# Kernel optimization log

Measured on AMD Instinct MI355X. Metric: run time of the kernel, lower is better.

Reference implementation:

```python
import jax, jax.numpy as jnp
import numpy as np
from functools import partial

N = 100000
E = 1600000
F_IN, F_HID, F_OUT = 128, 128, 64


def setup_inputs() -> dict:
    key = jax.random.key(0)
    ks = jax.random.split(key, 10)
    x = jax.random.normal(ks[0], (N, F_IN), dtype=jnp.float32)
    edge_index = jax.random.randint(ks[1], (2, E), 0, N, dtype=jnp.int64)
    edge_attr = jax.random.uniform(ks[2], (E,), dtype=jnp.float32)
    # GCNConv params: Linear(in, out, bias=False) weight + separate bias
    def glorot(k, fan_in, fan_out):
        lim = jnp.sqrt(6.0 / (fan_in + fan_out))
        return jax.random.uniform(k, (fan_in, fan_out), minval=-lim, maxval=lim, dtype=jnp.float32)
    return {
        "x": x, "edge_index": edge_index, "edge_attr": edge_attr,
        "W1": glorot(ks[3], F_IN, F_HID),  "b1": jnp.zeros((F_HID,), jnp.float32),
        "W2": glorot(ks[4], F_HID, F_HID), "b2": jnp.zeros((F_HID,), jnp.float32),
        "W3": glorot(ks[5], F_HID, F_OUT), "b3": jnp.zeros((F_OUT,), jnp.float32),
    }


def _gcn_norm(src, dst, ew, n):
    # PyG gcn_norm: add self-loops with weight 1, symmetric normalization.
    loop = jnp.arange(n, dtype=src.dtype)
    src_f = jnp.concatenate([src, loop])
    dst_f = jnp.concatenate([dst, loop])
    ew_f = jnp.concatenate([ew, jnp.ones((n,), ew.dtype)])
    deg = jax.ops.segment_sum(ew_f, dst_f, num_segments=n)
    dinv = jnp.where(deg > 0, jax.lax.rsqrt(deg), 0.0)
    norm = dinv[src_f] * ew_f * dinv[dst_f]  # [E+N]
    return src_f, dst_f, norm


def _gcn_conv(x, W, b, src_f, dst_f, norm, n):
    h = x @ W  # [N, out]
    msg = norm[:, None] * h[src_f]  # gather + per-edge scale
    out = jax.ops.segment_sum(msg, dst_f, num_segments=n)  # scatter-add
    return out + b


def reference(x, edge_index, edge_attr, W1, b1, W2, b2, W3, b3):
    n = x.shape[0]
    src, dst = edge_index[0], edge_index[1]
    src_f, dst_f, norm = _gcn_norm(src, dst, edge_attr, n)
    h = jax.nn.relu(_gcn_conv(x, W1, b1, src_f, dst_f, norm, n))
    h = jax.nn.relu(_gcn_conv(h, W2, b2, src_f, dst_f, norm, n))
    out = _gcn_conv(h, W3, b3, src_f, dst_f, norm, n)
    return jax.nn.log_softmax(out, axis=-1)
```

## Files before the change

kernel.cpp:

```cpp
#include <hip/hip_runtime.h>

typedef unsigned short ushortT;
typedef unsigned int uintT;
typedef unsigned long long ullT;
typedef __attribute__((ext_vector_type(8))) short bf16x8;
typedef __attribute__((ext_vector_type(4))) float f32x4;

#define NBUCK 391
#define EPB   4096
#define NBEB  391
#define BSLOT 4608
#define NCONV 3125

union H16 { ushortT u; _Float16 h; };

__device__ __forceinline__ float bf2f(uintT u16) {
    return __uint_as_float(u16 << 16);
}
__device__ __forceinline__ float bflo(uintT u) {
    return __uint_as_float(u << 16);
}
__device__ __forceinline__ float bfhi(uintT u) {
    return __uint_as_float(u & 0xffff0000u);
}
__device__ __forceinline__ ushortT f2bf(float f) {
    unsigned int u = __float_as_uint(f);
    unsigned int r = (u + 0x7fffu + ((u >> 16) & 1u)) >> 16;
    return (ushortT)r;
}

#define ACC8(U, W) \
    acc[0] = fmaf(W, bflo(U.x), acc[0]); acc[1] = fmaf(W, bfhi(U.x), acc[1]); \
    acc[2] = fmaf(W, bflo(U.y), acc[2]); acc[3] = fmaf(W, bfhi(U.y), acc[3]); \
    acc[4] = fmaf(W, bflo(U.z), acc[4]); acc[5] = fmaf(W, bfhi(U.z), acc[5]); \
    acc[6] = fmaf(W, bflo(U.w), acc[6]); acc[7] = fmaf(W, bfhi(U.w), acc[7]);


__device__ __forceinline__ void twist_body(const float* W, ushortT* Wt, int K, int C, int idx) {
    if (idx < K * C) {
        int k = idx / C, c = idx - k * C;
        Wt[c * K + k] = f2bf(W[idx]);
    }
}

__device__ __forceinline__ void conv_body(const float* x, ushortT* xb, int idx) {
    const float4* xp = reinterpret_cast<const float4*>(x) + (size_t)idx * 2;
    float4 a = xp[0], b = xp[1];
    uint4 o;
    o.x = (uintT)f2bf(a.x) | ((uintT)f2bf(a.y) << 16);
    o.y = (uintT)f2bf(a.z) | ((uintT)f2bf(a.w) << 16);
    o.z = (uintT)f2bf(b.x) | ((uintT)f2bf(b.y) << 16);
    o.w = (uintT)f2bf(b.z) | ((uintT)f2bf(b.w) << 16);
    *reinterpret_cast<uint4*>(xb + (size_t)idx * 8) = o;
}

template <int C>
__device__ __forceinline__ void gemm_body(const ushortT* A, const ushortT* Wt,
                                          ushortT* outp, int nrows, int bid, int tid) {
    const int K = 128;
    int wv = tid >> 6;
    int ln = tid & 63;
    int row0 = (bid * 4 + wv) * 16;
    if (row0 >= nrows) return;
    int rA = ln & 15;
    int kg = ln >> 4;
    int rowA = row0 + rA;
    bool okA = rowA < nrows;

    bf16x8 af[4];
    #pragma unroll
    for (int kb = 0; kb < 4; ++kb) {
        if (okA) af[kb] = *(const bf16x8*)(A + (size_t)rowA * K + kb * 32 + kg * 8);
        else     af[kb] = (bf16x8)(short)0;
    }

    int colB = ln & 15;
    f32x4 acc[C / 16];
    #pragma unroll
    for (int nt = 0; nt < C / 16; ++nt) acc[nt] = (f32x4)0.0f;
    #pragma unroll
    for (int nt = 0; nt < C / 16; ++nt) {
        int c = nt * 16 + colB;
        #pragma unroll
        for (int kb = 0; kb < 4; ++kb) {
            bf16x8 bfr = *(const bf16x8*)(Wt + c * K + kb * 32 + kg * 8);
            acc[nt] = __builtin_amdgcn_mfma_f32_16x16x32_bf16(af[kb], bfr, acc[nt], 0, 0, 0);
        }
    }
    #pragma unroll
    for (int nt = 0; nt < C / 16; ++nt) {
        #pragma unroll
        for (int r = 0; r < 4; ++r) {
            int rowC = row0 + (ln >> 4) * 4 + r;
            if (rowC < nrows) outp[(size_t)rowC * C + nt * 16 + colB] = f2bf(acc[nt][r]);
        }
    }
}

__global__ __launch_bounds__(512) void k_sort_twist(const int* src, const int* dst, const float* ew,
                                                    int* bucket_count, ullT* erec, int e,
                                                    const float* W1, ushortT* Wt1,
                                                    const float* W2, ushortT* Wt2,
                                                    const float* W3, ushortT* Wt3,
                                                    const float* x, ushortT* xb) {
    __shared__ ullT srec[EPB];
    __shared__ int  gaddr[EPB];
    __shared__ int  hist[512];
    __shared__ int  adj[NBUCK];
    int blk = blockIdx.x, t = threadIdx.x;
    if (blk >= NBEB) {
        int tb = blk - NBEB;
        if (tb < 32)      twist_body(W1, Wt1, 128, 128, tb * 512 + t);
        else if (tb < 64) twist_body(W2, Wt2, 128, 128, (tb - 32) * 512 + t);
        else if (tb < 80) twist_body(W3, Wt3, 128, 64, (tb - 64) * 512 + t);
        else              conv_body(x, xb, (tb - 80) * 512 + t);
        return;
    }
    hist[t] = 0;
    __syncthreads();
    int base = blk * EPB;
    for (int j = t; j < EPB; j += 512) {
        int i = base + j;
        if (i < e) atomicAdd(&hist[dst[i] >> 8], 1);
    }
    __syncthreads();
    int myc = hist[t];
    for (int off = 1; off < 512; off <<= 1) {
        int x2 = 0; if (t >= off) x2 = hist[t - off];
        __syncthreads();
        if (t >= off) hist[t] += x2;
        __syncthreads();
    }
    int lb = (t == 0) ? 0 : hist[t - 1];
    __syncthreads();
    hist[t] = lb;
    if (t < NBUCK) {
        int gb = 0;
        if (myc > 0) gb = atomicAdd(&bucket_count[t], myc);
        adj[t] = t * BSLOT + gb - lb;
    }
    __syncthreads();
    for (int j = t; j < EPB; j += 512) {
        int i = base + j;
        if (i < e) {
            int d = dst[i];
            int b = d >> 8;
            int pos = atomicAdd(&hist[b], 1);
            H16 cv; cv.h = (_Float16)ew[i];
            ullT rec = ((ullT)(uintT)src[i] << 24) | ((ullT)(uintT)(d & 255) << 16) | (ullT)cv.u;
            srec[pos] = rec;
            int ga = adj[b] + pos;
            int lim = b * BSLOT + BSLOT - 1;
            gaddr[pos] = ga <= lim ? ga : lim;
        }
    }
    __syncthreads();
    int m = e - base; if (m > EPB) m = EPB;
    for (int k = t; k < m; k += 512) {
        erec[(size_t)gaddr[k]] = srec[k];
    }
}

__global__ __launch_bounds__(256) void k_bucket_gemm1(const ullT* erec,
                                                      const int* bucket_count,
                                                      uintT* entries, float* dinv, int* counts, int n,
                                                      const ushortT* xb, const ushortT* Wt1,
                                                      ushortT* hw1) {
    __shared__ int cnt[256];
    __shared__ uintT wsum[256];
    int blk = blockIdx.x, t = threadIdx.x;
    if (blk < NBUCK) {
        int b = blk;
        cnt[t] = 0; wsum[t] = 0;
        __syncthreads();
        int beg = b * BSLOT, m = bucket_count[b];
        if (m > BSLOT) m = BSLOT;
        for (int j = t; j < m; j += 256) {
            ullT rec = erec[(size_t)beg + j];
            int dlow = (int)((rec >> 16) & 255);
            ushortT hu = (ushortT)(rec & 0xffffu);
            int slot = atomicAdd(&cnt[dlow], 1);
            H16 cv; cv.u = hu;
            atomicAdd(&wsum[dlow], (uintT)__float2uint_rn((float)cv.h * 16777216.0f));
            if (slot < 64) {
                uintT s = (uintT)(rec >> 24);
                entries[((size_t)b * 256 + dlow) * 64 + slot] = (s << 15) | (uintT)hu;
            }
        }
        __syncthreads();
        int node = b * 256 + t;
        if (node < n) {
            float sum = (float)wsum[t] * (1.0f / 16777216.0f);
            dinv[node] = rsqrtf(1.0f + sum);
            int c = cnt[t];
            counts[node] = c > 64 ? 64 : c;
        }
    } else {
        gemm_body<128>(xb, Wt1, hw1, n, blk - NBUCK, t);
    }
}

template <int C>
__global__ __launch_bounds__(256) void k_agg_gemm(const char* hwb, const float* dinv,
                                                  const int* counts, const uintT* entries,
                                                  const float* bias, const ushortT* Wt,
                                                  ushortT* outp, int n) {
    __shared__ ullT wp[4][64];
    __shared__ uintT rows[16][64];
    int wv = threadIdx.x >> 6, ln = threadIdx.x & 63;
    int tile0 = blockIdx.x * 16;
    int lg = ln & 15;
    int gp = ln >> 4;

    float wfac4[4], wsrc4[4];
    int   cnt4[4];
    uintT ent4[4];
    #pragma unroll
    for (int nn = 0; nn < 4; ++nn) {
        int i = tile0 + wv * 4 + nn;
        wfac4[nn] = dinv[i];
        cnt4[nn]  = counts[i];
        ent4[nn]  = entries[(size_t)i * 64 + ln];
        wsrc4[nn] = dinv[(int)(ent4[nn] >> 15)];
    }

    const char* lane_base = hwb + (size_t)(lg * 16);

    #pragma unroll
    for (int nn = 0; nn < 4; ++nn) {
        int r = wv * 4 + nn;
        int i = tile0 + r;
        float wfac = wfac4[nn];
        int cnt = cnt4[nn];
        int cntp = (cnt + 7) & ~7;
        uintT ent = ent4[nn];
        H16 cv; cv.u = (ushortT)(ent & 0x7fffu);
        float w_l = (ln < cnt) ? wsrc4[nn] * (float)cv.h * wfac : 0.f;
        uintT soff = (ln < cnt) ? ((ent >> 15) << 8) : 0u;
        wp[wv][ln] = ((ullT)__float_as_uint(w_l) << 32) | (ullT)soff;
        const ullT* wpw = wp[wv];

        uint4 uself = *(const uint4*)(lane_base + (size_t)i * 256);

        float acc[8];
        #pragma unroll
        for (int j = 0; j < 8; ++j) acc[j] = 0.f;

        ullT pa = wpw[gp], pb = wpw[4 + gp];
        uint4 ua = *(const uint4*)(lane_base + (uintT)pa);
        uint4 ub = *(const uint4*)(lane_base + (uintT)pb);
        for (int e = 8; e < cntp; e += 8) {
            ullT pa2 = wpw[e + gp], pb2 = wpw[e + 4 + gp];
            uint4 ua2 = *(const uint4*)(lane_base + (uintT)pa2);
            uint4 ub2 = *(const uint4*)(lane_base + (uintT)pb2);
            float wa = __uint_as_float((uintT)(pa >> 32));
            float wb = __uint_as_float((uintT)(pb >> 32));
            ACC8(ua, wa)
            ACC8(ub, wb)
            pa = pa2; pb = pb2; ua = ua2; ub = ub2;
        }
        {
            float wa = __uint_as_float((uintT)(pa >> 32));
            float wb = __uint_as_float((uintT)(pb >> 32));
            ACC8(ua, wa)
            ACC8(ub, wb)
        }

        #pragma unroll
        for (int j = 0; j < 8; ++j) {
            acc[j] += __shfl_xor(acc[j], 16);
            acc[j] += __shfl_xor(acc[j], 32);
        }
        float selfw = wfac * wfac;
        ACC8(uself, selfw)

        float a0 = (gp & 1) ? ((gp & 2) ? acc[6] : acc[2]) : ((gp & 2) ? acc[4] : acc[0]);
        float a1 = (gp & 1) ? ((gp & 2) ? acc[7] : acc[3]) : ((gp & 2) ? acc[5] : acc[1]);
        int d = lg * 4 + gp;
        float2 bs = *(const float2*)(bias + 2 * d);
        a0 = fmaxf(a0 + bs.x, 0.f);
        a1 = fmaxf(a1 + bs.y, 0.f);
        uintT packed = (uintT)f2bf(a0) | ((uintT)f2bf(a1) << 16);
        rows[r][((d * 4) ^ ((r & 7) << 4)) >> 2] = packed;
    }
    __syncthreads();

    {
        int rA = ln & 15;
        int kg = ln >> 4;
        int colB = ln & 15;
        const char* rbase = (const char*)&rows[0][0];
        bf16x8 af[4];
        #pragma unroll
        for (int kb = 0; kb < 4; ++kb) {
            int byteoff = (kb * 64 + kg * 16) ^ ((rA & 7) << 4);
            af[kb] = *(const bf16x8*)(rbase + rA * 256 + byteoff);
        }
        const int NS = C / 64;
        #pragma unroll
        for (int s = 0; s < NS; ++s) {
            int nt = wv * NS + s;
            f32x4 gac = (f32x4)0.0f;
            int c = nt * 16 + colB;
            #pragma unroll
            for (int kb = 0; kb < 4; ++kb) {
                bf16x8 bfr = *(const bf16x8*)(Wt + c * 128 + kb * 32 + kg * 8);
                gac = __builtin_amdgcn_mfma_f32_16x16x32_bf16(af[kb], bfr, gac, 0, 0, 0);
            }
            #pragma unroll
            for (int r = 0; r < 4; ++r) {
                int rowC = tile0 + kg * 4 + r;
                outp[(size_t)rowC * C + nt * 16 + colB] = f2bf(gac[r]);
            }
        }
    }
}

__global__ __launch_bounds__(256) void k_agg_softmax(const char* hwb, const float* dinv,
                                                     const int* counts, const uintT* entries,
                                                     const float* bias, float* outp, int n) {
    __shared__ ullT wp[4][64];
    int wv = threadIdx.x >> 6, ln = threadIdx.x & 63;
    int i = blockIdx.x * 4 + wv;
    if (i >= n) return;
    int lg = ln & 7;
    int gp = ln >> 3;

    float wfac = dinv[i];
    int cnt = counts[i];
    int cntp = (cnt + 7) & ~7;
    uintT ent = entries[(size_t)i * 64 + ln];
    int s_l = (ln < cnt) ? (int)(ent >> 15) : 0;
    H16 cv; cv.u = (ushortT)(ent & 0x7fffu);
    float w_l = (ln < cnt) ? dinv[s_l] * (float)cv.h * wfac : 0.f;
    wp[wv][ln] = ((ullT)__float_as_uint(w_l) << 32) | (ullT)((uintT)s_l << 7);
    const ullT* wpw = wp[wv];

    const char* lane_base = hwb + (size_t)(lg * 16);
    uint4 uself = *(const uint4*)(lane_base + (size_t)i * 128);

    float acc[8];
    #pragma unroll
    for (int j = 0; j < 8; ++j) acc[j] = 0.f;

    ullT paA = wpw[gp];
    uint4 uaA = *(const uint4*)(lane_base + (uintT)paA);
    bool hasB = cntp > 8;
    ullT paB = 0;
    uint4 uaB = {0, 0, 0, 0};
    if (hasB) {
        paB = wpw[8 + gp];
        uaB = *(const uint4*)(lane_base + (uintT)paB);
    }
    for (int e = 16; e < cntp; e += 8) {
        ullT paC = wpw[e + gp];
        uint4 uaC = *(const uint4*)(lane_base + (uintT)paC);
        float wa = __uint_as_float((uintT)(paA >> 32));
        ACC8(uaA, wa)
        paA = paB; uaA = uaB;
        paB = paC; uaB = uaC;
    }
    {
        float wa = __uint_as_float((uintT)(paA >> 32));
        ACC8(uaA, wa)
    }
    if (hasB) {
        float wa = __uint_as_float((uintT)(paB >> 32));
        ACC8(uaB, wa)
    }

    #pragma unroll
    for (int j = 0; j < 8; ++j) {
        acc[j] += __shfl_xor(acc[j], 8);
        acc[j] += __shfl_xor(acc[j], 16);
        acc[j] += __shfl_xor(acc[j], 32);
    }
    float selfw = wfac * wfac;
    ACC8(uself, selfw)

    float4 bsa = *(const float4*)(bias + lg * 8);
    float4 bsb = *(const float4*)(bias + lg * 8 + 4);
    acc[0] += bsa.x; acc[1] += bsa.y; acc[2] += bsa.z; acc[3] += bsa.w;
    acc[4] += bsb.x; acc[5] += bsb.y; acc[6] += bsb.z; acc[7] += bsb.w;

    float m = acc[0];
    #pragma unroll
    for (int j = 1; j < 8; ++j) m = fmaxf(m, acc[j]);
    m = fmaxf(m, __shfl_xor(m, 1));
    m = fmaxf(m, __shfl_xor(m, 2));
    m = fmaxf(m, __shfl_xor(m, 4));
    float s = 0.f;
    #pragma unroll
    for (int j = 0; j < 8; ++j) s += __expf(acc[j] - m);
    s += __shfl_xor(s, 1);
    s += __shfl_xor(s, 2);
    s += __shfl_xor(s, 4);
    float ls = m + __logf(s);

    float v0 = (gp & 1) ? acc[4] : acc[0];
    float v1 = (gp & 1) ? acc[5] : acc[1];
    float v2 = (gp & 1) ? acc[6] : acc[2];
    float v3 = (gp & 1) ? acc[7] : acc[3];
    if (gp < 2) {
        float4 r = { v0 - ls, v1 - ls, v2 - ls, v3 - ls };
        *(float4*)(outp + (size_t)i * 64 + lg * 8 + gp * 4) = r;
    }
}

extern "C" void kernel_launch(void* const* d_in, const int* in_sizes, int n_in,
                              void* d_out, int out_size, void* d_ws, size_t ws_size,
                              hipStream_t stream) {
    const int N = 100000, E = 1600000;
    const int NPAD = NBUCK * 256;
    const float* x  = (const float*)d_in[0];
    const int*   src = (const int*)d_in[1];
    const int*   dst = src + E;
    const float* ea = (const float*)d_in[2];
    const float* W1 = (const float*)d_in[3];
    const float* b1 = (const float*)d_in[4];
    const float* W2 = (const float*)d_in[5];
    const float* b2 = (const float*)d_in[6];
    const float* W3 = (const float*)d_in[7];
    const float* b3 = (const float*)d_in[8];
    float* outp = (float*)d_out;

    char* ws = (char*)d_ws;
    auto alloc = [&](size_t bytes) {
        char* p = ws;
        ws += (bytes + 255) & ~(size_t)255;
        return p;
    };
    int*   bucket_count = (int*)alloc((size_t)NBUCK * 4);
    ullT*  erec         = (ullT*)alloc((size_t)NBUCK * BSLOT * 8);
    float* dinv    = (float*)alloc((size_t)N * 4);
    int*   counts  = (int*)  alloc((size_t)N * 4);
    uintT* entries = (uintT*)alloc((size_t)NPAD * 64 * 4);
    ushortT* Wt1   = (ushortT*)alloc(128 * 128 * 2);
    ushortT* Wt2   = (ushortT*)alloc(128 * 128 * 2);
    ushortT* Wt3   = (ushortT*)alloc(128 * 64 * 2);
    ushortT* hwA   = (ushortT*)alloc((size_t)N * 128 * 2);
    ushortT* hwB   = (ushortT*)alloc((size_t)N * 128 * 2);
    ushortT* xb    = hwB;

    const int nbGemm = (N + 63) / 64;
    const int nbFused = N / 16;
    const int nbAgg  = (N + 3) / 4;

    hipMemsetAsync(bucket_count, 0, (size_t)NBUCK * 4, stream);
    k_sort_twist<<<NBEB + 80 + NCONV, 512, 0, stream>>>(src, dst, ea, bucket_count, erec, E,
                                                        W1, Wt1, W2, Wt2, W3, Wt3, x, xb);
    k_bucket_gemm1<<<NBUCK + nbGemm, 256, 0, stream>>>(erec, bucket_count,
                                                       entries, dinv, counts, N,
                                                       xb, Wt1, hwA);
    k_agg_gemm<128><<<nbFused, 256, 0, stream>>>((const char*)hwA, dinv, counts, entries,
                                                 b1, Wt2, hwB, N);
    k_agg_gemm<64><<<nbFused, 256, 0, stream>>>((const char*)hwB, dinv, counts, entries,
                                                b2, Wt3, hwA, N);
    k_agg_softmax<<<nbAgg, 256, 0, stream>>>((const char*)hwA, dinv, counts, entries,
                                             b3, outp, N);
}
```

Measured before the change: 358.9 us.

## Halve agg-gemm block to 2 waves with 8 nodes each and rolling prefetch

The fused aggregate+GEMM kernel now runs with 128 threads (2 wavefronts) per 16-node tile instead of 256, so each wave aggregates 8 nodes and computes twice as many MFMA output column tiles. The up-front load of per-node metadata for all nodes is replaced by a non-unrolled loop that prefetches the next node's dinv, count and entries while processing the current one, which reduces register pressure. The bias load is also hoisted out of the loop. The intent is higher occupancy and less redundant setup, at the cost of fewer waves per tile to hide gather latency.

New measurement: 368.2 us. +2.6%, slower.

```diff
diff --git a/kernel.cpp b/kernel.cpp
--- a/kernel.cpp
+++ b/kernel.cpp
@@ -201,41 +201,43 @@
 }
 
 template <int C>
-__global__ __launch_bounds__(256) void k_agg_gemm(const char* hwb, const float* dinv,
+__global__ __launch_bounds__(128) void k_agg_gemm(const char* hwb, const float* dinv,
                                                   const int* counts, const uintT* entries,
                                                   const float* bias, const ushortT* Wt,
                                                   ushortT* outp, int n) {
-    __shared__ ullT wp[4][64];
+    __shared__ ullT wp[2][64];
     __shared__ uintT rows[16][64];
     int wv = threadIdx.x >> 6, ln = threadIdx.x & 63;
     int tile0 = blockIdx.x * 16;
     int lg = ln & 15;
     int gp = ln >> 4;
 
-    float wfac4[4], wsrc4[4];
-    int   cnt4[4];
-    uintT ent4[4];
-    #pragma unroll
-    for (int nn = 0; nn < 4; ++nn) {
-        int i = tile0 + wv * 4 + nn;
-        wfac4[nn] = dinv[i];
-        cnt4[nn]  = counts[i];
-        ent4[nn]  = entries[(size_t)i * 64 + ln];
-        wsrc4[nn] = dinv[(int)(ent4[nn] >> 15)];
-    }
-
     const char* lane_base = hwb + (size_t)(lg * 16);
-
-    #pragma unroll
-    for (int nn = 0; nn < 4; ++nn) {
-        int r = wv * 4 + nn;
+    float2 bs = *(const float2*)(bias + 2 * (lg * 4 + gp));
+
+    int nd0 = wv * 8;
+    float wfac_n = dinv[tile0 + nd0];
+    int   cnt_n  = counts[tile0 + nd0];
+    uintT ent_n  = entries[(size_t)(tile0 + nd0) * 64 + ln];
+    float wsrc_n = dinv[(int)(ent_n >> 15)];
+
+    #pragma unroll 1
+    for (int nn = 0; nn < 8; ++nn) {
+        int r = nd0 + nn;
         int i = tile0 + r;
-        float wfac = wfac4[nn];
-        int cnt = cnt4[nn];
+        float wfac = wfac_n;
+        int cnt = cnt_n;
+        uintT ent = ent_n;
+        float wsrc = wsrc_n;
+        if (nn < 7) {
+            wfac_n = dinv[i + 1];
+            cnt_n  = counts[i + 1];
+            ent_n  = entries[(size_t)(i + 1) * 64 + ln];
+            wsrc_n = dinv[(int)(ent_n >> 15)];
+        }
         int cntp = (cnt + 7) & ~7;
-        uintT ent = ent4[nn];
         H16 cv; cv.u = (ushortT)(ent & 0x7fffu);
-        float w_l = (ln < cnt) ? wsrc4[nn] * (float)cv.h * wfac : 0.f;
+        float w_l = (ln < cnt) ? wsrc * (float)cv.h * wfac : 0.f;
         uintT soff = (ln < cnt) ? ((ent >> 15) << 8) : 0u;
         wp[wv][ln] = ((ullT)__float_as_uint(w_l) << 32) | (ullT)soff;
         const ullT* wpw = wp[wv];
@@ -276,12 +278,10 @@
 
         float a0 = (gp & 1) ? ((gp & 2) ? acc[6] : acc[2]) : ((gp & 2) ? acc[4] : acc[0]);
         float a1 = (gp & 1) ? ((gp & 2) ? acc[7] : acc[3]) : ((gp & 2) ? acc[5] : acc[1]);
-        int d = lg * 4 + gp;
-        float2 bs = *(const float2*)(bias + 2 * d);
         a0 = fmaxf(a0 + bs.x, 0.f);
         a1 = fmaxf(a1 + bs.y, 0.f);
         uintT packed = (uintT)f2bf(a0) | ((uintT)f2bf(a1) << 16);
-        rows[r][((d * 4) ^ ((r & 7) << 4)) >> 2] = packed;
+        rows[r][(((lg * 4 + gp) * 4) ^ ((r & 7) << 4)) >> 2] = packed;
     }
     __syncthreads();
 
@@ -296,7 +296,7 @@
             int byteoff = (kb * 64 + kg * 16) ^ ((rA & 7) << 4);
             af[kb] = *(const bf16x8*)(rbase + rA * 256 + byteoff);
         }
-        const int NS = C / 64;
+        const int NS = C / 32;
         #pragma unroll
         for (int s = 0; s < NS; ++s) {
             int nt = wv * NS + s;
@@ -452,9 +452,9 @@
     k_bucket_gemm1<<<NBUCK + nbGemm, 256, 0, stream>>>(erec, bucket_count,
                                                        entries, dinv, counts, N,
                                                        xb, Wt1, hwA);
-    k_agg_gemm<128><<<nbFused, 256, 0, stream>>>((const char*)hwA, dinv, counts, entries,
+    k_agg_gemm<128><<<nbFused, 128, 0, stream>>>((const char*)hwA, dinv, counts, entries,
                                                  b1, Wt2, hwB, N);
-    k_agg_gemm<64><<<nbFused, 256, 0, stream>>>((const char*)hwB, dinv, counts, entries,
+    k_agg_gemm<64><<<nbFused, 128, 0, stream>>>((const char*)hwB, dinv, counts, entries,
                                                 b2, Wt3, hwA, N);
     k_agg_softmax<<<nbAgg, 256, 0, stream>>>((const char*)hwA, dinv, counts, entries,
                                              b3, outp, N);
```
